# Kernel tuning notes

Hardware: AMD Instinct MI355X
Metric: run time of the kernel (lower is better)

The kernel has to match this reference:

```python
import jax, jax.numpy as jnp
import numpy as np

N = 100000
E = 3200000
C = 40
L_CORR = 10
L_SMOOTH = 10
ALPHA_CORR = 0.979
ALPHA_SMOOTH = 0.756


def setup_inputs() -> dict:
    key = jax.random.key(0)
    k1, k2, k3, k4 = jax.random.split(key, 4)
    y_true = jax.random.randint(k1, (N,), 0, C, dtype=jnp.int32)
    y_soft = jax.random.uniform(k2, (N, C), dtype=jnp.float32)
    y_soft = y_soft / y_soft.sum(axis=1, keepdims=True)
    spread_mask = jax.random.randint(k3, (N,), 0, 2, dtype=jnp.int32).astype(bool)
    edge_index = jax.random.randint(k4, (2, E), 0, N, dtype=jnp.int32)
    return {"y_true": y_true, "y_soft": y_soft, "spread_mask": spread_mask,
            "edge_index": edge_index}


def _gcn_norm(src, dst, n):
    # symmetric normalization D^-1/2 A D^-1/2 from the edge list
    deg = jax.ops.segment_sum(jnp.ones_like(dst, dtype=jnp.float32), dst,
                              num_segments=n)
    dinv = jnp.where(deg > 0, jax.lax.rsqrt(jnp.maximum(deg, 1.0)), 0.0)
    return dinv[src] * dinv[dst]  # [E]


def _label_prop(y0, src, dst, norm, n, alpha, n_layers, post_step):
    # out <- post_step(alpha * A_hat @ out + (1 - alpha) * y0), repeated
    def body(_, out):
        agg = jax.ops.segment_sum(out[src] * norm[:, None], dst,
                                  num_segments=n)  # [N, C]
        return post_step(alpha * agg + (1.0 - alpha) * y0)
    return jax.lax.fori_loop(0, n_layers, body, y0)


def _correct_and_smooth(y_true, y_soft, spread_mask, edge_index):
    src, dst = edge_index[0], edge_index[1]
    norm = _gcn_norm(src, dst, N)
    onehot = jax.nn.one_hot(y_true, C, dtype=y_soft.dtype)  # [N, C]
    m = spread_mask[:, None]

    # ---- correct: propagate masked residual error, autoscale path ----
    error = jnp.where(m, onehot - y_soft, 0.0)
    smoothed_error = _label_prop(error, src, dst, norm, N, ALPHA_CORR,
                                 L_CORR, lambda x: jnp.clip(x, -1.0, 1.0))
    numel = jnp.sum(spread_mask).astype(y_soft.dtype)
    sigma = jnp.sum(jnp.abs(error)) / numel  # error is zero off-mask
    denom = jnp.sum(jnp.abs(smoothed_error), axis=1, keepdims=True)
    scale = sigma / denom  # [N, 1]
    scale = jnp.where(jnp.isinf(scale) | (scale > 1000.0), 1.0, scale)
    y_corr = y_soft + scale * smoothed_error

    # ---- smooth: inject true labels on spread_mask, propagate w/ softmax ----
    y0 = jnp.where(m, onehot, y_corr)
    out = _label_prop(y0, src, dst, norm, N, ALPHA_SMOOTH, L_SMOOTH,
                      lambda x: jax.nn.softmax(x, axis=-1))
    return out


def reference(y_true, y_soft, spread_mask, edge_index):
    return _correct_and_smooth(y_true, y_soft, spread_mask, edge_index)
```

## Files before the change

kernel.cpp:

```cpp
#include <hip/hip_runtime.h>
#include <hip/hip_fp16.h>
#include <math.h>

#define C 40

__global__ void k_detect(const unsigned int* __restrict__ w, int nwords,
                         unsigned int* __restrict__ flags) {
    int i = blockIdx.x * blockDim.x + threadIdx.x;
    unsigned int viol = 0;
    for (; i < nwords; i += gridDim.x * blockDim.x) {
        unsigned int v = w[i];
        if (!(v == 0u || v == 1u)) viol |= 1u;
        if (!(v == 0u || v == 0x3F800000u)) viol |= 2u;
    }
    if (viol) atomicOr(flags, viol);
}

__device__ __forceinline__ bool read_mask(const void* mp, unsigned int fl, int n) {
    if ((fl & 1u) == 0u) return ((const int*)mp)[n] != 0;
    if ((fl & 2u) == 0u) return ((const float*)mp)[n] != 0.0f;
    return ((const unsigned char*)mp)[n] != 0;
}

__global__ void k_deg(const int* __restrict__ dst, int* __restrict__ deg, int E) {
    int i = blockIdx.x * blockDim.x + threadIdx.x;
    if (i < E) atomicAdd(&deg[dst[i]], 1);
}

__global__ void k_dinv(const int* __restrict__ deg, float* __restrict__ dinv, int n) {
    int i = blockIdx.x * blockDim.x + threadIdx.x;
    if (i < n) {
        int d = deg[i];
        dinv[i] = (d > 0) ? rsqrtf((float)d) : 0.0f;
    }
}

__global__ void k_scan1(const int* __restrict__ in, int* __restrict__ outp,
                        int* __restrict__ bsum, int n) {
    __shared__ int sm[256];
    int tid = threadIdx.x;
    int i = blockIdx.x * 256 + tid;
    int v = (i < n) ? in[i] : 0;
    sm[tid] = v;
    __syncthreads();
#pragma unroll
    for (int o = 1; o < 256; o <<= 1) {
        int t = (tid >= o) ? sm[tid - o] : 0;
        __syncthreads();
        sm[tid] += t;
        __syncthreads();
    }
    if (i <= n) outp[i] = sm[tid] - v;
    if (tid == 255) bsum[blockIdx.x] = sm[255];
}

__global__ void k_scan2(int* __restrict__ bsum, int nb) {
    __shared__ int sm[512];
    int tid = threadIdx.x;
    int v = (tid < nb) ? bsum[tid] : 0;
    sm[tid] = v;
    __syncthreads();
    for (int o = 1; o < 512; o <<= 1) {
        int t = (tid >= o) ? sm[tid - o] : 0;
        __syncthreads();
        sm[tid] += t;
        __syncthreads();
    }
    if (tid < nb) bsum[tid] = sm[tid] - v;
}

__global__ void k_scan3(int* __restrict__ outp, const int* __restrict__ bsum, int n) {
    int i = blockIdx.x * 256 + threadIdx.x;
    if (i <= n) outp[i] += bsum[blockIdx.x];
}

__global__ void k_csr(const int* __restrict__ src, const int* __restrict__ dst,
                      const float* __restrict__ dinv, const int* __restrict__ rowptr,
                      int* __restrict__ fill, unsigned long long* __restrict__ pk,
                      int E) {
    int e = blockIdx.x * blockDim.x + threadIdx.x;
    if (e < E) {
        int s = src[e], d = dst[e];
        int pos = rowptr[d] + atomicAdd(&fill[d], 1);
        unsigned long long u = (unsigned)s |
            ((unsigned long long)(unsigned)__float_as_int(dinv[s] * dinv[d]) << 32);
        pk[pos] = u;
    }
}

__global__ __launch_bounds__(256) void k_error(
    const float4* __restrict__ ys4, const int* __restrict__ y_true,
    const void* __restrict__ maskp, const unsigned int* __restrict__ flags,
    char* __restrict__ err, float* __restrict__ psig, float* __restrict__ pcnt,
    int n) {
    unsigned int fl = *flags;
    unsigned boff = (unsigned)n * 64u;
    float a = 0.f, cnt = 0.f;
    int nq = n * 10;
    for (int i = blockIdx.x * blockDim.x + threadIdx.x; i < nq;
         i += gridDim.x * blockDim.x) {
        int node = i / 10;
        int q = i - node * 10;
        float e0 = 0.f, e1 = 0.f, e2 = 0.f, e3 = 0.f;
        if (read_mask(maskp, fl, node)) {
            int yt = y_true[node];
            float4 ys = ys4[i];
            int c0 = q * 4;
            e0 = ((c0 + 0) == yt ? 1.f : 0.f) - ys.x;
            e1 = ((c0 + 1) == yt ? 1.f : 0.f) - ys.y;
            e2 = ((c0 + 2) == yt ? 1.f : 0.f) - ys.z;
            e3 = ((c0 + 3) == yt ? 1.f : 0.f) - ys.w;
            a += fabsf(e0) + fabsf(e1) + fabsf(e2) + fabsf(e3);
            if (q == 0) cnt += 1.f;
        }
        __half2 h01 = __floats2half2_rn(e0, e1);
        __half2 h23 = __floats2half2_rn(e2, e3);
        uint2 w;
        w.x = *(unsigned*)&h01;
        w.y = *(unsigned*)&h23;
        unsigned off = (q < 8) ? (unsigned)node * 64u + (unsigned)q * 8u
                               : boff + (unsigned)node * 16u + (unsigned)(q - 8) * 8u;
        *(uint2*)(err + off) = w;
    }
    __shared__ float sA[256];
    __shared__ float sB[256];
    int tid = threadIdx.x;
    sA[tid] = a; sB[tid] = cnt;
    __syncthreads();
    for (int o = 128; o; o >>= 1) {
        if (tid < o) { sA[tid] += sA[tid + o]; sB[tid] += sB[tid + o]; }
        __syncthreads();
    }
    if (tid == 0) { psig[blockIdx.x] = sA[0]; pcnt[blockIdx.x] = sB[0]; }
}

__global__ __launch_bounds__(256) void k_reduce(
    const float* __restrict__ psig, const float* __restrict__ pcnt,
    float* __restrict__ s_sig, float* __restrict__ s_cnt, int nb) {
    float a = 0.f, c = 0.f;
    for (int i = threadIdx.x; i < nb; i += 256) { a += psig[i]; c += pcnt[i]; }
    __shared__ float sA[256];
    __shared__ float sB[256];
    int tid = threadIdx.x;
    sA[tid] = a; sB[tid] = c;
    __syncthreads();
    for (int o = 128; o; o >>= 1) {
        if (tid < o) { sA[tid] += sA[tid + o]; sB[tid] += sB[tid + o]; }
        __syncthreads();
    }
    if (tid == 0) { *s_sig = sA[0]; *s_cnt = sB[0]; }
}

#define PKLOAD(U, EE)                                                        \
    _Pragma("unroll") for (int j = 0; j < GRP; ++j) { U[j] = pk8[(EE) + j]; }

#define GATH(XV, U)                                                          \
    _Pragma("unroll") for (int j = 0; j < GRP; ++j) {                        \
        unsigned s = (unsigned)(U[j] & 0xffffffffu);                         \
        XV[j] = *(const __half*)(xc + ((s << shift) + aoff));                \
    }

#define FMAG(U, XV)                                                          \
    _Pragma("unroll") for (int j = 0; j < GRP; ++j) {                        \
        acc[j & 3] = fmaf(__int_as_float((int)(U[j] >> 32)),                 \
                          __half2float(XV[j]), acc[j & 3]);                  \
    }

template <int POST, int F32OUT>
__global__ __launch_bounds__(256) void k_prop(
    const int* __restrict__ rowptr, const unsigned long long* __restrict__ pk8,
    const char* __restrict__ xc, const char* __restrict__ y0,
    void* __restrict__ outv, float alpha, float beta, int n) {
    int wid = (blockIdx.x * blockDim.x + threadIdx.x) >> 6;
    int lane = threadIdx.x & 63;
    if (wid >= n) return;
    int beg = __builtin_amdgcn_readfirstlane(rowptr[wid]);
    int end = __builtin_amdgcn_readfirstlane(rowptr[wid + 1]);
    bool isA = (lane < 32);
    unsigned shift = isA ? 6u : 4u;
    unsigned aoff = isA ? (unsigned)(lane * 2)
                        : (unsigned)n * 64u + (unsigned)((lane - 32) * 2);

    float y0v = __half2float(*(const __half*)(y0 + (((unsigned)wid << shift) + aoff)));
    float acc[4] = {0.f, 0.f, 0.f, 0.f};
    int e = beg;
    {
        enum { GRP = 16 };
        for (; e + GRP <= end; e += GRP) {
            unsigned long long u[GRP];
            __half xv[GRP];
            PKLOAD(u, e)
            GATH(xv, u)
            FMAG(u, xv)
        }
    }
    {
        enum { GRP = 8 };
        if (e + GRP <= end) {
            unsigned long long u[GRP];
            __half xv[GRP];
            PKLOAD(u, e)
            GATH(xv, u)
            FMAG(u, xv)
            e += GRP;
        }
    }
    for (; e < end; ++e) {
        unsigned long long u = pk8[e];
        unsigned s = (unsigned)(u & 0xffffffffu);
        float xv = __half2float(*(const __half*)(xc + ((s << shift) + aoff)));
        acc[0] = fmaf(__int_as_float((int)(u >> 32)), xv, acc[0]);
    }
    float a = (acc[0] + acc[1]) + (acc[2] + acc[3]);
    float v = fmaf(alpha, a, beta * y0v);

    float res;
    if (POST == 0) {
        res = fminf(1.0f, fmaxf(-1.0f, v));
    } else {
        float mx = (lane < C) ? v : -3.0e38f;
#pragma unroll
        for (int o = 32; o; o >>= 1) mx = fmaxf(mx, __shfl_xor(mx, o));
        float ex = (lane < C) ? __expf(v - mx) : 0.0f;
        float s = ex;
#pragma unroll
        for (int o = 32; o; o >>= 1) s += __shfl_xor(s, o);
        res = ex / s;
    }
    if (lane < C) {
        if (F32OUT) {
            ((float*)outv)[(size_t)wid * C + lane] = res;
        } else {
            *(__half*)((char*)outv + (((unsigned)wid << shift) + aoff)) =
                __float2half(res);
        }
    }
}

__global__ __launch_bounds__(256) void k_scale(
    const char* __restrict__ sm_err, const float* __restrict__ y_soft,
    const int* __restrict__ y_true, const void* __restrict__ maskp,
    const unsigned int* __restrict__ flags, const float* __restrict__ s_sig,
    const float* __restrict__ s_cnt, char* __restrict__ y0, int n) {
    int wid = (blockIdx.x * blockDim.x + threadIdx.x) >> 6;
    int lane = threadIdx.x & 63;
    if (wid >= n) return;
    bool isA = (lane < 32);
    unsigned shift = isA ? 6u : 4u;
    unsigned aoff = isA ? (unsigned)(lane * 2)
                        : (unsigned)n * 64u + (unsigned)((lane - 32) * 2);
    float v = 0.f, a = 0.f;
    if (lane < C) {
        v = __half2float(*(const __half*)(sm_err + (((unsigned)wid << shift) + aoff)));
        a = fabsf(v);
    }
#pragma unroll
    for (int o = 32; o; o >>= 1) a += __shfl_xor(a, o);
    float sigma = (*s_sig) / (*s_cnt);
    float scale = sigma / a;
    if (isinf(scale) || scale > 1000.0f) scale = 1.0f;
    if (lane < C) {
        bool m = read_mask(maskp, *flags, wid);
        float yc = fmaf(scale, v, y_soft[(size_t)wid * C + lane]);
        float r = m ? ((lane == y_true[wid]) ? 1.0f : 0.0f) : yc;
        *(__half*)(y0 + (((unsigned)wid << shift) + aoff)) = __float2half(r);
    }
}

extern "C" void kernel_launch(void* const* d_in, const int* in_sizes, int n_in,
                              void* d_out, int out_size, void* d_ws, size_t ws_size,
                              hipStream_t stream) {
    const int* y_true = (const int*)d_in[0];
    const float* y_soft = (const float*)d_in[1];
    const void* maskp = d_in[2];
    const int* ei = (const int*)d_in[3];
    const int n = in_sizes[0];
    const int E = in_sizes[3] / 2;
    const int* src = ei;
    const int* dst = ei + E;

    char* ws = (char*)d_ws;
    size_t off = 0;
    auto alloc = [&](size_t bytes) -> char* {
        char* p = ws + off;
        off += (bytes + 255) & ~(size_t)255;
        return p;
    };
    int* deg = (int*)alloc((size_t)n * 4);
    int* fill = (int*)alloc((size_t)n * 4);
    unsigned int* flags = (unsigned int*)alloc(4);
    size_t zero_bytes = off;
    float* s_sig = (float*)alloc(4);
    float* s_cnt = (float*)alloc(4);
    float* psig = (float*)alloc(2048 * 4);
    float* pcnt = (float*)alloc(2048 * 4);
    float* dinv = (float*)alloc((size_t)n * 4);
    int* rowptr = (int*)alloc((size_t)(n + 1) * 4);
    int* bsum = (int*)alloc(4096);
    unsigned long long* pk = (unsigned long long*)alloc((size_t)E * 8);
    size_t fb = (size_t)n * 80 + 512;
    char* hE = alloc(fb);
    char* hY = alloc(fb);
    char* hA = alloc(fb);
    char* hB = alloc(fb);
    (void)ws_size;

    hipMemsetAsync(d_ws, 0, zero_bytes, stream);

    k_detect<<<98, 256, 0, stream>>>((const unsigned int*)maskp, n / 4, flags);
    k_deg<<<(E + 255) / 256, 256, 0, stream>>>(dst, deg, E);
    k_dinv<<<(n + 255) / 256, 256, 0, stream>>>(deg, dinv, n);

    int nb1 = (n + 1 + 255) / 256;
    k_scan1<<<nb1, 256, 0, stream>>>(deg, rowptr, bsum, n);
    k_scan2<<<1, 512, 0, stream>>>(bsum, nb1);
    k_scan3<<<nb1, 256, 0, stream>>>(rowptr, bsum, n);
    k_csr<<<(E + 255) / 256, 256, 0, stream>>>(src, dst, dinv, rowptr, fill, pk, E);

    k_error<<<2048, 256, 0, stream>>>((const float4*)y_soft, y_true, maskp, flags,
                                      hE, psig, pcnt, n);
    k_reduce<<<1, 256, 0, stream>>>(psig, pcnt, s_sig, s_cnt, 2048);

    const int pb = (n + 3) / 4;
    const float A1 = 0.979f, B1 = (float)(1.0 - 0.979);
    const float A2 = 0.756f, B2 = (float)(1.0 - 0.756);
    char* bufs[2] = { hA, hB };

    const char* x = hE;
    for (int it = 0; it < 10; ++it) {
        k_prop<0, 0><<<pb, 256, 0, stream>>>(rowptr, pk, x, hE, bufs[it & 1], A1, B1, n);
        x = bufs[it & 1];
    }
    k_scale<<<pb, 256, 0, stream>>>(x, y_soft, y_true, maskp, flags, s_sig, s_cnt, hY, n);

    x = hY;
    for (int it = 0; it < 9; ++it) {
        k_prop<1, 0><<<pb, 256, 0, stream>>>(rowptr, pk, x, hY, bufs[it & 1], A2, B2, n);
        x = bufs[it & 1];
    }
    k_prop<1, 1><<<pb, 256, 0, stream>>>(rowptr, pk, x, hY, d_out, A2, B2, n);
}
```

Measured before the change: 1.602 ms.

## Gather 8-byte feature chunks per lane with shuffle-broadcast edge lists in SpMM

The propagation kernel stops having every lane gather a single half per edge. Each wavefront now loads a block of 16 packed edges once, coalesced, and broadcasts sources and weights with shuffles. Each 8-lane group then gathers 8-byte (4-half) chunks of a source row and handles a different edge, so there are fewer, wider memory transactions per edge. Partial sums are combined across lane groups with xor-shuffle reductions and redistributed to channel lanes, which adds shuffle overhead.

```diff
diff --git a/kernel.cpp b/kernel.cpp
--- a/kernel.cpp
+++ b/kernel.cpp
@@ -151,24 +151,22 @@
     if (tid == 0) { *s_sig = sA[0]; *s_cnt = sB[0]; }
 }
 
-#define PKLOAD(U, EE)                                                        \
-    _Pragma("unroll") for (int j = 0; j < GRP; ++j) { U[j] = pk8[(EE) + j]; }
-
-#define GATH(XV, U)                                                          \
-    _Pragma("unroll") for (int j = 0; j < GRP; ++j) {                        \
-        unsigned s = (unsigned)(U[j] & 0xffffffffu);                         \
-        XV[j] = *(const __half*)(xc + ((s << shift) + aoff));                \
-    }
-
-#define FMAG(U, XV)                                                          \
-    _Pragma("unroll") for (int j = 0; j < GRP; ++j) {                        \
-        acc[j & 3] = fmaf(__int_as_float((int)(U[j] >> 32)),                 \
-                          __half2float(XV[j]), acc[j & 3]);                  \
+#define FMA4(ACC, NB, XV)                                                    \
+    {                                                                        \
+        float nrm_ = __int_as_float(NB);                                     \
+        __half2 h01_ = *(__half2*)&(XV).x;                                   \
+        __half2 h23_ = *(__half2*)&(XV).y;                                   \
+        float2 f01_ = __half22float2(h01_);                                  \
+        float2 f23_ = __half22float2(h23_);                                  \
+        ACC[0] = fmaf(nrm_, f01_.x, ACC[0]);                                 \
+        ACC[1] = fmaf(nrm_, f01_.y, ACC[1]);                                 \
+        ACC[2] = fmaf(nrm_, f23_.x, ACC[2]);                                 \
+        ACC[3] = fmaf(nrm_, f23_.y, ACC[3]);                                 \
     }
 
 template <int POST, int F32OUT>
 __global__ __launch_bounds__(256) void k_prop(
-    const int* __restrict__ rowptr, const unsigned long long* __restrict__ pk8,
+    const int* __restrict__ rowptr, const int* __restrict__ pkw,
     const char* __restrict__ xc, const char* __restrict__ y0,
     void* __restrict__ outv, float alpha, float beta, int n) {
     int wid = (blockIdx.x * blockDim.x + threadIdx.x) >> 6;
@@ -176,43 +174,89 @@
     if (wid >= n) return;
     int beg = __builtin_amdgcn_readfirstlane(rowptr[wid]);
     int end = __builtin_amdgcn_readfirstlane(rowptr[wid + 1]);
+    int g = lane >> 3;
+    unsigned cl8 = (unsigned)(lane & 7) << 3;
+    unsigned p8 = (unsigned)(lane & 1) << 3;
+    unsigned boff = (unsigned)n << 6;
     bool isA = (lane < 32);
     unsigned shift = isA ? 6u : 4u;
-    unsigned aoff = isA ? (unsigned)(lane * 2)
-                        : (unsigned)n * 64u + (unsigned)((lane - 32) * 2);
+    unsigned aoff = isA ? (unsigned)(lane * 2) : boff + (unsigned)((lane - 32) * 2);
 
     float y0v = __half2float(*(const __half*)(y0 + (((unsigned)wid << shift) + aoff)));
-    float acc[4] = {0.f, 0.f, 0.f, 0.f};
+
+    float accA[4] = {0.f, 0.f, 0.f, 0.f};
+    float accB[4] = {0.f, 0.f, 0.f, 0.f};
+    float tacc = 0.f;
     int e = beg;
-    {
-        enum { GRP = 16 };
-        for (; e + GRP <= end; e += GRP) {
-            unsigned long long u[GRP];
-            __half xv[GRP];
-            PKLOAD(u, e)
-            GATH(xv, u)
-            FMAG(u, xv)
+    for (; e + 16 <= end; e += 16) {
+        int w = 0;
+        if (lane < 32) w = pkw[2 * e + lane];
+        int s0 = __shfl(w, 2 * g);
+        int nb0 = __shfl(w, 2 * g + 1);
+        int s1 = __shfl(w, 16 + 2 * g);
+        int nb1 = __shfl(w, 16 + 2 * g + 1);
+        uint2 a0 = *(const uint2*)(xc + (((unsigned)s0 << 6) + cl8));
+        uint2 a1 = *(const uint2*)(xc + (((unsigned)s1 << 6) + cl8));
+        FMA4(accA, nb0, a0)
+        FMA4(accA, nb1, a1)
+        if (lane < 32) {
+            int sB = __shfl(w, lane & 30);
+            int nbB = __shfl(w, (lane & 30) + 1);
+            uint2 b0 = *(const uint2*)(xc + (boff + ((unsigned)sB << 4) + p8));
+            FMA4(accB, nbB, b0)
         }
     }
-    {
-        enum { GRP = 8 };
-        if (e + GRP <= end) {
-            unsigned long long u[GRP];
-            __half xv[GRP];
-            PKLOAD(u, e)
-            GATH(xv, u)
-            FMAG(u, xv)
-            e += GRP;
+    if (e + 8 <= end) {
+        int w = 0;
+        if (lane < 16) w = pkw[2 * e + lane];
+        int s0 = __shfl(w, 2 * g);
+        int nb0 = __shfl(w, 2 * g + 1);
+        uint2 a0 = *(const uint2*)(xc + (((unsigned)s0 << 6) + cl8));
+        FMA4(accA, nb0, a0)
+        if (lane < 16) {
+            int sB = __shfl(w, lane & 14);
+            int nbB = __shfl(w, (lane & 14) + 1);
+            uint2 b0 = *(const uint2*)(xc + (boff + ((unsigned)sB << 4) + p8));
+            FMA4(accB, nbB, b0)
         }
-    }
+        e += 8;
+    }
+    const unsigned long long* pk8 = (const unsigned long long*)pkw;
     for (; e < end; ++e) {
         unsigned long long u = pk8[e];
         unsigned s = (unsigned)(u & 0xffffffffu);
         float xv = __half2float(*(const __half*)(xc + ((s << shift) + aoff)));
-        acc[0] = fmaf(__int_as_float((int)(u >> 32)), xv, acc[0]);
-    }
-    float a = (acc[0] + acc[1]) + (acc[2] + acc[3]);
-    float v = fmaf(alpha, a, beta * y0v);
+        tacc = fmaf(__int_as_float((int)(u >> 32)), xv, tacc);
+    }
+#pragma unroll
+    for (int m = 8; m <= 32; m <<= 1) {
+        accA[0] += __shfl_xor(accA[0], m);
+        accA[1] += __shfl_xor(accA[1], m);
+        accA[2] += __shfl_xor(accA[2], m);
+        accA[3] += __shfl_xor(accA[3], m);
+    }
+#pragma unroll
+    for (int m = 2; m <= 16; m <<= 1) {
+        accB[0] += __shfl_xor(accB[0], m);
+        accB[1] += __shfl_xor(accB[1], m);
+        accB[2] += __shfl_xor(accB[2], m);
+        accB[3] += __shfl_xor(accB[3], m);
+    }
+    int q = lane >> 2;
+    float va0 = __shfl(accA[0], q);
+    float va1 = __shfl(accA[1], q);
+    float va2 = __shfl(accA[2], q);
+    float va3 = __shfl(accA[3], q);
+    int pB = q & 1;
+    float vb0 = __shfl(accB[0], pB);
+    float vb1 = __shfl(accB[1], pB);
+    float vb2 = __shfl(accB[2], pB);
+    float vb3 = __shfl(accB[3], pB);
+    int r = lane & 3;
+    float vA = (r & 2) ? ((r & 1) ? va3 : va2) : ((r & 1) ? va1 : va0);
+    float vB = (r & 2) ? ((r & 1) ? vb3 : vb2) : ((r & 1) ? vb1 : vb0);
+    float amain = isA ? vA : vB;
+    float v = fmaf(alpha, amain + tacc, beta * y0v);
 
     float res;
     if (POST == 0) {
@@ -325,18 +369,19 @@
     const float A1 = 0.979f, B1 = (float)(1.0 - 0.979);
     const float A2 = 0.756f, B2 = (float)(1.0 - 0.756);
     char* bufs[2] = { hA, hB };
+    const int* pkw = (const int*)pk;
 
     const char* x = hE;
     for (int it = 0; it < 10; ++it) {
-        k_prop<0, 0><<<pb, 256, 0, stream>>>(rowptr, pk, x, hE, bufs[it & 1], A1, B1, n);
+        k_prop<0, 0><<<pb, 256, 0, stream>>>(rowptr, pkw, x, hE, bufs[it & 1], A1, B1, n);
         x = bufs[it & 1];
     }
     k_scale<<<pb, 256, 0, stream>>>(x, y_soft, y_true, maskp, flags, s_sig, s_cnt, hY, n);
 
     x = hY;
     for (int it = 0; it < 9; ++it) {
-        k_prop<1, 0><<<pb, 256, 0, stream>>>(rowptr, pk, x, hY, bufs[it & 1], A2, B2, n);
+        k_prop<1, 0><<<pb, 256, 0, stream>>>(rowptr, pkw, x, hY, bufs[it & 1], A2, B2, n);
         x = bufs[it & 1];
     }
-    k_prop<1, 1><<<pb, 256, 0, stream>>>(rowptr, pk, x, hY, d_out, A2, B2, n);
-}
+    k_prop<1, 1><<<pb, 256, 0, stream>>>(rowptr, pkw, x, hY, d_out, A2, B2, n);
+}
```

Result: slower. 1.861 ms (+16.2%).

## Partition CSR build into destination ranges and use masked tail in gather

Applied to the files above, without the earlier changes.

The CSR fill now runs as 16 passes, each scattering only edges whose destination falls in one node range. This keeps the atomic counters and the packed-edge writes within a smaller region that can stay cache-resident, at the cost of reading src/dst 16 times. The propagation kernel replaces the 8-wide and scalar tail loops with one 16-wide masked tail that clamps indices and zeroes the weights of extra lanes. This keeps more loads in flight for short rows but issues redundant gathers.

```diff
diff --git a/kernel.cpp b/kernel.cpp
--- a/kernel.cpp
+++ b/kernel.cpp
@@ -77,14 +77,17 @@
 __global__ void k_csr(const int* __restrict__ src, const int* __restrict__ dst,
                       const float* __restrict__ dinv, const int* __restrict__ rowptr,
                       int* __restrict__ fill, unsigned long long* __restrict__ pk,
-                      int E) {
+                      int E, int lo, int hi) {
     int e = blockIdx.x * blockDim.x + threadIdx.x;
     if (e < E) {
-        int s = src[e], d = dst[e];
-        int pos = rowptr[d] + atomicAdd(&fill[d], 1);
-        unsigned long long u = (unsigned)s |
-            ((unsigned long long)(unsigned)__float_as_int(dinv[s] * dinv[d]) << 32);
-        pk[pos] = u;
+        int d = dst[e];
+        if (d >= lo && d < hi) {
+            int s = src[e];
+            int pos = rowptr[d] + atomicAdd(&fill[d], 1);
+            unsigned long long u = (unsigned)s |
+                ((unsigned long long)(unsigned)__float_as_int(dinv[s] * dinv[d]) << 32);
+            pk[pos] = u;
+        }
     }
 }
 
@@ -151,21 +154,6 @@
     if (tid == 0) { *s_sig = sA[0]; *s_cnt = sB[0]; }
 }
 
-#define PKLOAD(U, EE)                                                        \
-    _Pragma("unroll") for (int j = 0; j < GRP; ++j) { U[j] = pk8[(EE) + j]; }
-
-#define GATH(XV, U)                                                          \
-    _Pragma("unroll") for (int j = 0; j < GRP; ++j) {                        \
-        unsigned s = (unsigned)(U[j] & 0xffffffffu);                         \
-        XV[j] = *(const __half*)(xc + ((s << shift) + aoff));                \
-    }
-
-#define FMAG(U, XV)                                                          \
-    _Pragma("unroll") for (int j = 0; j < GRP; ++j) {                        \
-        acc[j & 3] = fmaf(__int_as_float((int)(U[j] >> 32)),                 \
-                          __half2float(XV[j]), acc[j & 3]);                  \
-    }
-
 template <int POST, int F32OUT>
 __global__ __launch_bounds__(256) void k_prop(
     const int* __restrict__ rowptr, const unsigned long long* __restrict__ pk8,
@@ -184,32 +172,40 @@
     float y0v = __half2float(*(const __half*)(y0 + (((unsigned)wid << shift) + aoff)));
     float acc[4] = {0.f, 0.f, 0.f, 0.f};
     int e = beg;
-    {
-        enum { GRP = 16 };
-        for (; e + GRP <= end; e += GRP) {
-            unsigned long long u[GRP];
-            __half xv[GRP];
-            PKLOAD(u, e)
-            GATH(xv, u)
-            FMAG(u, xv)
-        }
-    }
-    {
-        enum { GRP = 8 };
-        if (e + GRP <= end) {
-            unsigned long long u[GRP];
-            __half xv[GRP];
-            PKLOAD(u, e)
-            GATH(xv, u)
-            FMAG(u, xv)
-            e += GRP;
-        }
-    }
-    for (; e < end; ++e) {
-        unsigned long long u = pk8[e];
-        unsigned s = (unsigned)(u & 0xffffffffu);
-        float xv = __half2float(*(const __half*)(xc + ((s << shift) + aoff)));
-        acc[0] = fmaf(__int_as_float((int)(u >> 32)), xv, acc[0]);
+    for (; e + 16 <= end; e += 16) {
+        unsigned long long u[16];
+        __half xv[16];
+#pragma unroll
+        for (int j = 0; j < 16; ++j) u[j] = pk8[e + j];
+#pragma unroll
+        for (int j = 0; j < 16; ++j) {
+            unsigned s = (unsigned)(u[j] & 0xffffffffu);
+            xv[j] = *(const __half*)(xc + ((s << shift) + aoff));
+        }
+#pragma unroll
+        for (int j = 0; j < 16; ++j) {
+            acc[j & 3] = fmaf(__int_as_float((int)(u[j] >> 32)),
+                              __half2float(xv[j]), acc[j & 3]);
+        }
+    }
+    if (e < end) {
+        unsigned long long u[16];
+        __half xv[16];
+#pragma unroll
+        for (int j = 0; j < 16; ++j) {
+            int ec = e + j < end ? e + j : end - 1;
+            u[j] = pk8[ec];
+        }
+#pragma unroll
+        for (int j = 0; j < 16; ++j) {
+            unsigned s = (unsigned)(u[j] & 0xffffffffu);
+            xv[j] = *(const __half*)(xc + ((s << shift) + aoff));
+        }
+#pragma unroll
+        for (int j = 0; j < 16; ++j) {
+            float nrm = (e + j < end) ? __int_as_float((int)(u[j] >> 32)) : 0.0f;
+            acc[j & 3] = fmaf(nrm, __half2float(xv[j]), acc[j & 3]);
+        }
     }
     float a = (acc[0] + acc[1]) + (acc[2] + acc[3]);
     float v = fmaf(alpha, a, beta * y0v);
@@ -297,7 +293,7 @@
     float* dinv = (float*)alloc((size_t)n * 4);
     int* rowptr = (int*)alloc((size_t)(n + 1) * 4);
     int* bsum = (int*)alloc(4096);
-    unsigned long long* pk = (unsigned long long*)alloc((size_t)E * 8);
+    unsigned long long* pk = (unsigned long long*)alloc((size_t)E * 8 + 256);
     size_t fb = (size_t)n * 80 + 512;
     char* hE = alloc(fb);
     char* hY = alloc(fb);
@@ -315,7 +311,12 @@
     k_scan1<<<nb1, 256, 0, stream>>>(deg, rowptr, bsum, n);
     k_scan2<<<1, 512, 0, stream>>>(bsum, nb1);
     k_scan3<<<nb1, 256, 0, stream>>>(rowptr, bsum, n);
-    k_csr<<<(E + 255) / 256, 256, 0, stream>>>(src, dst, dinv, rowptr, fill, pk, E);
+    for (int p = 0; p < 16; ++p) {
+        int lo = (int)((long long)p * n / 16);
+        int hi = (int)((long long)(p + 1) * n / 16);
+        k_csr<<<(E + 255) / 256, 256, 0, stream>>>(src, dst, dinv, rowptr, fill,
+                                                   pk, E, lo, hi);
+    }
 
     k_error<<<2048, 256, 0, stream>>>((const float4*)y_soft, y_true, maskp, flags,
                                       hE, psig, pcnt, n);
```

After: 1.587 ms. Within noise of the previous version (-0.9%).

## Split wavefront into 6 edge groups with 4-wide channel gathers

Applied to the files above, without the earlier changes.

The propagation kernel now splits each 64-lane wavefront into six groups of ten lanes. Each group handles a different edge and each lane gathers four half-precision channels at once with 8-byte loads, then the partial sums are combined with shuffles. The previous kernel had one edge per wavefront iteration with 2-byte per-lane gathers. CSR construction also records each edge's slot during the degree atomic pass, so the second atomic pass is replaced by a plain indexed write. This costs an extra E-sized slot array and padding of the packed edge array.

```diff
diff --git a/kernel.cpp b/kernel.cpp
--- a/kernel.cpp
+++ b/kernel.cpp
@@ -22,9 +22,10 @@
     return ((const unsigned char*)mp)[n] != 0;
 }
 
-__global__ void k_deg(const int* __restrict__ dst, int* __restrict__ deg, int E) {
-    int i = blockIdx.x * blockDim.x + threadIdx.x;
-    if (i < E) atomicAdd(&deg[dst[i]], 1);
+__global__ void k_slot(const int* __restrict__ dst, int* __restrict__ fill,
+                       int* __restrict__ slots, int E) {
+    int e = blockIdx.x * blockDim.x + threadIdx.x;
+    if (e < E) slots[e] = atomicAdd(&fill[dst[e]], 1);
 }
 
 __global__ void k_dinv(const int* __restrict__ deg, float* __restrict__ dinv, int n) {
@@ -74,14 +75,14 @@
     if (i <= n) outp[i] += bsum[blockIdx.x];
 }
 
-__global__ void k_csr(const int* __restrict__ src, const int* __restrict__ dst,
-                      const float* __restrict__ dinv, const int* __restrict__ rowptr,
-                      int* __restrict__ fill, unsigned long long* __restrict__ pk,
-                      int E) {
+__global__ void k_wr(const int* __restrict__ src, const int* __restrict__ dst,
+                     const int* __restrict__ slots, const float* __restrict__ dinv,
+                     const int* __restrict__ rowptr,
+                     unsigned long long* __restrict__ pk, int E) {
     int e = blockIdx.x * blockDim.x + threadIdx.x;
     if (e < E) {
-        int s = src[e], d = dst[e];
-        int pos = rowptr[d] + atomicAdd(&fill[d], 1);
+        int d = dst[e], s = src[e];
+        int pos = rowptr[d] + slots[e];
         unsigned long long u = (unsigned)s |
             ((unsigned long long)(unsigned)__float_as_int(dinv[s] * dinv[d]) << 32);
         pk[pos] = u;
@@ -151,21 +152,6 @@
     if (tid == 0) { *s_sig = sA[0]; *s_cnt = sB[0]; }
 }
 
-#define PKLOAD(U, EE)                                                        \
-    _Pragma("unroll") for (int j = 0; j < GRP; ++j) { U[j] = pk8[(EE) + j]; }
-
-#define GATH(XV, U)                                                          \
-    _Pragma("unroll") for (int j = 0; j < GRP; ++j) {                        \
-        unsigned s = (unsigned)(U[j] & 0xffffffffu);                         \
-        XV[j] = *(const __half*)(xc + ((s << shift) + aoff));                \
-    }
-
-#define FMAG(U, XV)                                                          \
-    _Pragma("unroll") for (int j = 0; j < GRP; ++j) {                        \
-        acc[j & 3] = fmaf(__int_as_float((int)(U[j] >> 32)),                 \
-                          __half2float(XV[j]), acc[j & 3]);                  \
-    }
-
 template <int POST, int F32OUT>
 __global__ __launch_bounds__(256) void k_prop(
     const int* __restrict__ rowptr, const unsigned long long* __restrict__ pk8,
@@ -176,63 +162,92 @@
     if (wid >= n) return;
     int beg = __builtin_amdgcn_readfirstlane(rowptr[wid]);
     int end = __builtin_amdgcn_readfirstlane(rowptr[wid + 1]);
-    bool isA = (lane < 32);
-    unsigned shift = isA ? 6u : 4u;
-    unsigned aoff = isA ? (unsigned)(lane * 2)
-                        : (unsigned)n * 64u + (unsigned)((lane - 32) * 2);
-
-    float y0v = __half2float(*(const __half*)(y0 + (((unsigned)wid << shift) + aoff)));
-    float acc[4] = {0.f, 0.f, 0.f, 0.f};
-    int e = beg;
-    {
-        enum { GRP = 16 };
-        for (; e + GRP <= end; e += GRP) {
-            unsigned long long u[GRP];
-            __half xv[GRP];
-            PKLOAD(u, e)
-            GATH(xv, u)
-            FMAG(u, xv)
-        }
-    }
-    {
-        enum { GRP = 8 };
-        if (e + GRP <= end) {
-            unsigned long long u[GRP];
-            __half xv[GRP];
-            PKLOAD(u, e)
-            GATH(xv, u)
-            FMAG(u, xv)
-            e += GRP;
-        }
-    }
-    for (; e < end; ++e) {
-        unsigned long long u = pk8[e];
-        unsigned s = (unsigned)(u & 0xffffffffu);
-        float xv = __half2float(*(const __half*)(xc + ((s << shift) + aoff)));
-        acc[0] = fmaf(__int_as_float((int)(u >> 32)), xv, acc[0]);
-    }
-    float a = (acc[0] + acc[1]) + (acc[2] + acc[3]);
-    float v = fmaf(alpha, a, beta * y0v);
-
-    float res;
+    int j = lane / 10;
+    int k = lane - j * 10;
+    int jbig = (lane < 60) ? j : 0x40000000;
+    unsigned jo = (unsigned)(((lane < 60) ? j : 5) * 8);
+    unsigned shift = (k < 8) ? 6u : 4u;
+    unsigned off = (k < 8) ? (unsigned)(k * 8)
+                           : (unsigned)n * 64u + (unsigned)((k - 8) * 8);
+
+    uint2 yv = *(const uint2*)(y0 + (((unsigned)wid << shift) + off));
+    __half2 yh01 = *(__half2*)&yv.x;
+    __half2 yh23 = *(__half2*)&yv.y;
+    float2 yf01 = __half22float2(yh01);
+    float2 yf23 = __half22float2(yh23);
+
+    float a0 = 0.f, a1 = 0.f, a2 = 0.f, a3 = 0.f;
+    const char* pkc = (const char*)(pk8 + beg);
+    int rem = end - beg;
+    int t = 0;
+    for (; rem > 0; rem -= 12, t += 12) {
+        unsigned long long ua = *(const unsigned long long*)(pkc + (size_t)t * 8 + jo);
+        unsigned long long ub = *(const unsigned long long*)(pkc + (size_t)(t + 6) * 8 + jo);
+        unsigned sa = (unsigned)(ua & 0xffffffffu);
+        unsigned sb = (unsigned)(ub & 0xffffffffu);
+        uint2 xa = *(const uint2*)(xc + ((sa << shift) + off));
+        uint2 xb = *(const uint2*)(xc + ((sb << shift) + off));
+        float na = (jbig < rem) ? __int_as_float((int)(ua >> 32)) : 0.0f;
+        float nb = (jbig < rem - 6) ? __int_as_float((int)(ub >> 32)) : 0.0f;
+        __half2 ha01 = *(__half2*)&xa.x;
+        __half2 ha23 = *(__half2*)&xa.y;
+        float2 fa01 = __half22float2(ha01);
+        float2 fa23 = __half22float2(ha23);
+        a0 = fmaf(na, fa01.x, a0); a1 = fmaf(na, fa01.y, a1);
+        a2 = fmaf(na, fa23.x, a2); a3 = fmaf(na, fa23.y, a3);
+        __half2 hb01 = *(__half2*)&xb.x;
+        __half2 hb23 = *(__half2*)&xb.y;
+        float2 fb01 = __half22float2(hb01);
+        float2 fb23 = __half22float2(hb23);
+        a0 = fmaf(nb, fb01.x, a0); a1 = fmaf(nb, fb01.y, a1);
+        a2 = fmaf(nb, fb23.x, a2); a3 = fmaf(nb, fb23.y, a3);
+    }
+
+    a0 += __shfl(a0, lane + 30); a1 += __shfl(a1, lane + 30);
+    a2 += __shfl(a2, lane + 30); a3 += __shfl(a3, lane + 30);
+    float t0a = __shfl(a0, lane + 10), t1a = __shfl(a1, lane + 10);
+    float t2a = __shfl(a2, lane + 10), t3a = __shfl(a3, lane + 10);
+    float t0b = __shfl(a0, lane + 20), t1b = __shfl(a1, lane + 20);
+    float t2b = __shfl(a2, lane + 20), t3b = __shfl(a3, lane + 20);
+    a0 += t0a + t0b; a1 += t1a + t1b; a2 += t2a + t2b; a3 += t3a + t3b;
+
+    float v0 = fmaf(alpha, a0, beta * yf01.x);
+    float v1 = fmaf(alpha, a1, beta * yf01.y);
+    float v2 = fmaf(alpha, a2, beta * yf23.x);
+    float v3 = fmaf(alpha, a3, beta * yf23.y);
+
+    bool valid = (lane < 10);
+    float r0, r1, r2, r3;
     if (POST == 0) {
-        res = fminf(1.0f, fmaxf(-1.0f, v));
+        r0 = fminf(1.0f, fmaxf(-1.0f, v0));
+        r1 = fminf(1.0f, fmaxf(-1.0f, v1));
+        r2 = fminf(1.0f, fmaxf(-1.0f, v2));
+        r3 = fminf(1.0f, fmaxf(-1.0f, v3));
     } else {
-        float mx = (lane < C) ? v : -3.0e38f;
+        float mx = valid ? fmaxf(fmaxf(v0, v1), fmaxf(v2, v3)) : -3.0e38f;
 #pragma unroll
-        for (int o = 32; o; o >>= 1) mx = fmaxf(mx, __shfl_xor(mx, o));
-        float ex = (lane < C) ? __expf(v - mx) : 0.0f;
-        float s = ex;
+        for (int o = 8; o; o >>= 1) mx = fmaxf(mx, __shfl_xor(mx, o));
+        float e0 = valid ? __expf(v0 - mx) : 0.f;
+        float e1 = valid ? __expf(v1 - mx) : 0.f;
+        float e2 = valid ? __expf(v2 - mx) : 0.f;
+        float e3 = valid ? __expf(v3 - mx) : 0.f;
+        float ss = (e0 + e1) + (e2 + e3);
 #pragma unroll
-        for (int o = 32; o; o >>= 1) s += __shfl_xor(s, o);
-        res = ex / s;
-    }
-    if (lane < C) {
+        for (int o = 8; o; o >>= 1) ss += __shfl_xor(ss, o);
+        float inv = 1.0f / ss;
+        r0 = e0 * inv; r1 = e1 * inv; r2 = e2 * inv; r3 = e3 * inv;
+    }
+
+    if (valid) {
         if (F32OUT) {
-            ((float*)outv)[(size_t)wid * C + lane] = res;
+            ((float4*)outv)[(size_t)wid * 10 + k] = make_float4(r0, r1, r2, r3);
         } else {
-            *(__half*)((char*)outv + (((unsigned)wid << shift) + aoff)) =
-                __float2half(res);
+            __half2 h01 = __floats2half2_rn(r0, r1);
+            __half2 h23 = __floats2half2_rn(r2, r3);
+            uint2 w;
+            w.x = *(unsigned*)&h01;
+            w.y = *(unsigned*)&h23;
+            *(uint2*)((char*)outv + (((unsigned)wid << shift) + off)) = w;
         }
     }
 }
@@ -286,7 +301,6 @@
         off += (bytes + 255) & ~(size_t)255;
         return p;
     };
-    int* deg = (int*)alloc((size_t)n * 4);
     int* fill = (int*)alloc((size_t)n * 4);
     unsigned int* flags = (unsigned int*)alloc(4);
     size_t zero_bytes = off;
@@ -297,7 +311,8 @@
     float* dinv = (float*)alloc((size_t)n * 4);
     int* rowptr = (int*)alloc((size_t)(n + 1) * 4);
     int* bsum = (int*)alloc(4096);
-    unsigned long long* pk = (unsigned long long*)alloc((size_t)E * 8);
+    int* slots = (int*)alloc((size_t)E * 4);
+    unsigned long long* pk = (unsigned long long*)alloc(((size_t)E + 32) * 8);
     size_t fb = (size_t)n * 80 + 512;
     char* hE = alloc(fb);
     char* hY = alloc(fb);
@@ -306,16 +321,17 @@
     (void)ws_size;
 
     hipMemsetAsync(d_ws, 0, zero_bytes, stream);
+    hipMemsetAsync(pk + E, 0, 32 * 8, stream);
 
     k_detect<<<98, 256, 0, stream>>>((const unsigned int*)maskp, n / 4, flags);
-    k_deg<<<(E + 255) / 256, 256, 0, stream>>>(dst, deg, E);
-    k_dinv<<<(n + 255) / 256, 256, 0, stream>>>(deg, dinv, n);
+    k_slot<<<(E + 255) / 256, 256, 0, stream>>>(dst, fill, slots, E);
+    k_dinv<<<(n + 255) / 256, 256, 0, stream>>>(fill, dinv, n);
 
     int nb1 = (n + 1 + 255) / 256;
-    k_scan1<<<nb1, 256, 0, stream>>>(deg, rowptr, bsum, n);
+    k_scan1<<<nb1, 256, 0, stream>>>(fill, rowptr, bsum, n);
     k_scan2<<<1, 512, 0, stream>>>(bsum, nb1);
     k_scan3<<<nb1, 256, 0, stream>>>(rowptr, bsum, n);
-    k_csr<<<(E + 255) / 256, 256, 0, stream>>>(src, dst, dinv, rowptr, fill, pk, E);
+    k_wr<<<(E + 255) / 256, 256, 0, stream>>>(src, dst, slots, dinv, rowptr, pk, E);
 
     k_error<<<2048, 256, 0, stream>>>((const float4*)y_soft, y_true, maskp, flags,
                                       hE, psig, pcnt, n);
```

Measured after the change: 1.502 ms. -6.2%, faster.
